# Kernel tuning notes

Measured on AMD Instinct MI355X. Metric: run time of the kernel, lower is better.

The kernel has to match this reference:

```python
import jax, jax.numpy as jnp
import numpy as np

NEG_SLOPE = 0.2
LN_EPS = 1e-5


def gat_conv(x, edge_index, W, att_src, att_dst, bias, heads, out_ch, concat):
    """PyG-style GATConv with add_self_loops=True, eval mode (no dropout)."""
    N = x.shape[0]
    loop = jnp.arange(N, dtype=edge_index.dtype)
    src = jnp.concatenate([edge_index[0], loop])
    dst = jnp.concatenate([edge_index[1], loop])
    h = (x @ W).reshape(N, heads, out_ch)                      # [N,H,C]
    a_src = jnp.sum(h * att_src, axis=-1)                      # [N,H]
    a_dst = jnp.sum(h * att_dst, axis=-1)                      # [N,H]
    e = jax.nn.leaky_relu(a_src[src] + a_dst[dst], NEG_SLOPE)  # [E,H]
    emax = jax.ops.segment_max(e, dst, num_segments=N)         # [N,H]
    ex = jnp.exp(e - emax[dst])
    denom = jax.ops.segment_sum(ex, dst, num_segments=N)       # [N,H]
    alpha = ex / denom[dst]                                    # [E,H]
    msg = h[src] * alpha[..., None]                            # [E,H,C]
    out = jax.ops.segment_sum(msg, dst, num_segments=N)        # [N,H,C]
    out = out.reshape(N, heads * out_ch) if concat else out.mean(axis=1)
    return out + bias


def layer_norm(x, w, b):
    mu = x.mean(-1, keepdims=True)
    var = jnp.mean((x - mu) ** 2, -1, keepdims=True)
    return (x - mu) * jax.lax.rsqrt(var + LN_EPS) * w + b


def setup_inputs() -> dict:
    key = jax.random.key(0)
    ks = jax.random.split(key, 16)
    N, E, R = 50000, 800000, 16
    node_dim, res_dim, hidden, heads = 128, 64, 64, 2
    s = lambda fan: 1.0 / np.sqrt(fan)
    return {
        "x": jax.random.normal(ks[0], (N, node_dim), jnp.float32),
        "edge_index": jax.random.randint(ks[1], (2, E), 0, N, jnp.int64),
        "resource_features": jax.random.normal(ks[2], (N, R, res_dim), jnp.float32),
        "W1": jax.random.normal(ks[3], (node_dim, heads * hidden), jnp.float32) * s(node_dim),
        "att_src1": jax.random.normal(ks[4], (heads, hidden), jnp.float32) * s(hidden),
        "att_dst1": jax.random.normal(ks[5], (heads, hidden), jnp.float32) * s(hidden),
        "b1": jnp.zeros((heads * hidden,), jnp.float32),
        "W2": jax.random.normal(ks[6], (heads * hidden, hidden), jnp.float32) * s(heads * hidden),
        "att_src2": jax.random.normal(ks[7], (1, hidden), jnp.float32) * s(hidden),
        "att_dst2": jax.random.normal(ks[8], (1, hidden), jnp.float32) * s(hidden),
        "b2": jnp.zeros((hidden,), jnp.float32),
        "ln_w": jnp.ones((hidden,), jnp.float32),
        "ln_b": jnp.zeros((hidden,), jnp.float32),
        "res_W": jax.random.normal(ks[9], (res_dim, hidden), jnp.float32) * s(res_dim),
        "res_b": jnp.zeros((hidden,), jnp.float32),
    }


def reference(x, edge_index, resource_features, W1, att_src1, att_dst1, b1,
              W2, att_src2, att_dst2, b2, ln_w, ln_b, res_W, res_b):
    hidden = W2.shape[1]
    heads = att_src1.shape[0]
    h = jax.nn.elu(gat_conv(x, edge_index, W1, att_src1, att_dst1, b1,
                            heads, hidden, concat=True))
    h = gat_conv(h, edge_index, W2, att_src2, att_dst2, b2,
                 1, hidden, concat=False)
    h = layer_norm(h, ln_w, ln_b)                              # [N, hidden]
    R = resource_features.shape[1]
    x_expanded = jnp.broadcast_to(h[:, None, :], (h.shape[0], R, hidden))
    res_emb = jax.nn.elu(resource_features @ res_W + res_b)    # [N,R,hidden]
    return jnp.concatenate([x_expanded, res_emb], axis=-1)     # [N,R,2*hidden]
```

## Files before the change

### kernel.cpp

```cpp
#include <hip/hip_runtime.h>
#include <hip/hip_bf16.h>
#include <math.h>

#define LEAKY_SLOPE 0.2f
#define LN_EPS 1e-5f

typedef __attribute__((ext_vector_type(4))) float f32x4;
typedef __attribute__((ext_vector_type(8))) short short8;

__device__ __forceinline__ float leaky_relu(float x) { return x >= 0.f ? x : LEAKY_SLOPE * x; }
__device__ __forceinline__ float elu1(float x) { return x > 0.f ? x : expm1f(x); }
__device__ __forceinline__ short f2bf(float f) {
    union { __hip_bfloat16 b; short s; } u;
    u.b = __float2bfloat16(f);
    return u.s;
}
__device__ __forceinline__ float bflo(unsigned u) { union { unsigned i; float f; } x; x.i = u << 16; return x.f; }
__device__ __forceinline__ float bfhi(unsigned u) { union { unsigned i; float f; } x; x.i = u & 0xffff0000u; return x.f; }
__device__ __forceinline__ float sbf(short s) { union { unsigned i; float f; } x; x.i = ((unsigned)(unsigned short)s) << 16; return x.f; }
__device__ __forceinline__ unsigned fkey(float f) {
    unsigned b = __float_as_uint(f);
    return b ^ (unsigned)(((int)b >> 31) | 0x80000000);
}
__device__ __forceinline__ float funkey(unsigned k) {
    unsigned b = (k & 0x80000000u) ? (k ^ 0x80000000u) : ~k;
    return __uint_as_float(b);
}

#define DETECT_IS64(ei, E)                                              \
    __shared__ int s_is64;                                              \
    {                                                                   \
        if (threadIdx.x < 64) {                                         \
            int v = (threadIdx.x < (E)) ? ((const int*)(ei))[2 * threadIdx.x + 1] : 0; \
            unsigned long long b = __ballot(v != 0);                    \
            if (threadIdx.x == 0) s_is64 = (b == 0ULL);                 \
        }                                                               \
        __syncthreads();                                                \
    }

#define SUBW1 130
#define DEGB 512
__global__ __launch_bounds__(256) void k_fat1(
    const float* __restrict__ x, const float* __restrict__ W1,
    const float* __restrict__ att_s, const float* __restrict__ att_d,
    short* __restrict__ h1, float* __restrict__ a_src, float* __restrict__ a_dst,
    unsigned* __restrict__ amax, int N,
    const void* __restrict__ ei, int E, int* __restrict__ deg,
    const float* __restrict__ resW, short* __restrict__ rwb, int nbG)
{
    if ((int)blockIdx.x >= nbG) {
        const int b0 = (int)blockIdx.x - nbG;
        if (b0 == 0) {
            for (int idx = threadIdx.x; idx < 4096; idx += 256) {
                int f = idx >> 9, lane = (idx >> 3) & 63, j = idx & 7;
                int kk = f >> 2, nc = f & 3;
                int k = kk * 32 + (lane >> 4) * 8 + j;
                int col = nc * 16 + (lane & 15);
                rwb[idx] = f2bf(resW[k * 64 + col]);
            }
        }
        DETECT_IS64(ei, E)
        const int is64 = s_is64;
        for (int e = b0 * 256 + threadIdx.x; e < E; e += DEGB * 256) {
            int d = is64 ? (int)((const long long*)ei)[(size_t)E + e] : ((const int*)ei)[(size_t)E + e];
            atomicAdd(&deg[d], 1);
        }
        return;
    }
    __shared__ short WT[16 * SUBW1 * 8];
    __shared__ float sb[64 * 4];
    __shared__ float wm[8];
    const int t = threadIdx.x;
    const int w = t >> 6, l = t & 63, lr = l & 15, lk = l >> 4;
    const int n0 = blockIdx.x * 64;
    for (int idx = t; idx < 16384; idx += 256) {
        int k = idx >> 7, col = idx & 127;
        WT[((k >> 3) * SUBW1 + col) * 8 + (k & 7)] = f2bf(W1[idx]);
    }
    sb[t] = 0.f;
    __syncthreads();

    f32x4 acc[4][2];
    #pragma unroll
    for (int mt = 0; mt < 4; ++mt)
        #pragma unroll
        for (int nt = 0; nt < 2; ++nt) acc[mt][nt] = (f32x4){0.f, 0.f, 0.f, 0.f};

    #pragma unroll
    for (int ks = 0; ks < 4; ++ks) {
        short8 bfr[2];
        #pragma unroll
        for (int nt = 0; nt < 2; ++nt) {
            int col = w * 32 + nt * 16 + lr;
            int kk = ks * 4 + lk;
            bfr[nt] = *(const short8*)&WT[(kk * SUBW1 + col) * 8];
        }
        #pragma unroll
        for (int mt = 0; mt < 4; ++mt) {
            int row = n0 + mt * 16 + lr; if (row >= N) row = N - 1;
            const float* ap = x + (size_t)row * 128 + ks * 32 + lk * 8;
            float4 u0 = *(const float4*)ap;
            float4 u1 = *(const float4*)(ap + 4);
            short8 af;
            af[0] = f2bf(u0.x); af[1] = f2bf(u0.y); af[2] = f2bf(u0.z); af[3] = f2bf(u0.w);
            af[4] = f2bf(u1.x); af[5] = f2bf(u1.y); af[6] = f2bf(u1.z); af[7] = f2bf(u1.w);
            acc[mt][0] = __builtin_amdgcn_mfma_f32_16x16x32_bf16(af, bfr[0], acc[mt][0], 0, 0, 0);
            acc[mt][1] = __builtin_amdgcn_mfma_f32_16x16x32_bf16(af, bfr[1], acc[mt][1], 0, 0, 0);
        }
    }

    const int head = w >> 1;
    float asv[2], adv[2];
    #pragma unroll
    for (int nt = 0; nt < 2; ++nt) {
        int ci = (w & 1) * 32 + nt * 16 + lr;
        asv[nt] = att_s[head * 64 + ci];
        adv[nt] = att_d[head * 64 + ci];
    }
    #pragma unroll
    for (int mt = 0; mt < 4; ++mt) {
        #pragma unroll
        for (int i = 0; i < 4; ++i) {
            float ps = acc[mt][0][i] * asv[0] + acc[mt][1][i] * asv[1];
            float pd = acc[mt][0][i] * adv[0] + acc[mt][1][i] * adv[1];
            #pragma unroll
            for (int o = 1; o < 16; o <<= 1) { ps += __shfl_xor(ps, o); pd += __shfl_xor(pd, o); }
            int rl = mt * 16 + lk * 4 + i;
            if (lr == 0) {
                atomicAdd(&sb[rl * 4 + head], ps);
                atomicAdd(&sb[rl * 4 + 2 + head], pd);
            }
            int row = n0 + rl;
            if (row < N) {
                h1[(size_t)row * 128 + w * 32 + lr]      = f2bf(acc[mt][0][i]);
                h1[(size_t)row * 128 + w * 32 + 16 + lr] = f2bf(acc[mt][1][i]);
            }
        }
    }
    __syncthreads();
    int nl = t >> 2, q = t & 3, n = n0 + nl;
    float v = sb[t];
    bool ok = (n < N);
    if (ok) {
        if (q == 0) a_src[n * 2 + 0] = v;
        else if (q == 1) a_src[n * 2 + 1] = v;
        else if (q == 2) a_dst[n * 2 + 0] = v;
        else a_dst[n * 2 + 1] = v;
    }
    float m0 = (ok && q == 0) ? v : -1e30f;
    float m1 = (ok && q == 1) ? v : -1e30f;
    #pragma unroll
    for (int o = 32; o; o >>= 1) { m0 = fmaxf(m0, __shfl_xor(m0, o)); m1 = fmaxf(m1, __shfl_xor(m1, o)); }
    if (l == 0) { wm[w] = m0; wm[4 + w] = m1; }
    __syncthreads();
    if (t == 0) {
        float M0 = fmaxf(fmaxf(wm[0], wm[1]), fmaxf(wm[2], wm[3]));
        float M1 = fmaxf(fmaxf(wm[4], wm[5]), fmaxf(wm[6], wm[7]));
        atomicMax(&amax[0], fkey(M0));
        atomicMax(&amax[1], fkey(M1));
    }
}

__global__ __launch_bounds__(256) void k_bsum(const int* __restrict__ deg, int* __restrict__ bsum, int n)
{
    __shared__ int ws[4];
    const int base = blockIdx.x * 1024;
    int s = 0;
    for (int j = threadIdx.x; j < 1024; j += 256) {
        int i = base + j;
        s += (i < n) ? deg[i] : 0;
    }
    #pragma unroll
    for (int o = 32; o; o >>= 1) s += __shfl_down(s, o);
    if ((threadIdx.x & 63) == 0) ws[threadIdx.x >> 6] = s;
    __syncthreads();
    if (threadIdx.x == 0) bsum[blockIdx.x] = ws[0] + ws[1] + ws[2] + ws[3];
}

__global__ void k_scanb(const int* __restrict__ bsum, int* __restrict__ bbase, int nb)
{
    const int l = threadIdx.x;
    int carry = 0;
    for (int b = 0; b < nb; b += 64) {
        int v = (b + l < nb) ? bsum[b + l] : 0;
        int x = v;
        #pragma unroll
        for (int o = 1; o < 64; o <<= 1) { int y = __shfl_up(x, o); if (l >= o) x += y; }
        if (b + l < nb) bbase[b + l] = carry + x - v;
        carry += __shfl(x, 63);
    }
}

__global__ __launch_bounds__(1024) void k_scan3(const int* __restrict__ deg, const int* __restrict__ bbase,
                                                int* __restrict__ offs, int* __restrict__ cursor, int n)
{
    __shared__ int ws[16];
    const int i = blockIdx.x * 1024 + threadIdx.x;
    const int l = threadIdx.x & 63, w = threadIdx.x >> 6;
    int v = (i < n) ? deg[i] : 0;
    int x = v;
    #pragma unroll
    for (int o = 1; o < 64; o <<= 1) { int y = __shfl_up(x, o); if (l >= o) x += y; }
    if (l == 63) ws[w] = x;
    __syncthreads();
    if (threadIdx.x < 16) {
        int s = ws[threadIdx.x];
        #pragma unroll
        for (int o = 1; o < 16; o <<= 1) { int y = __shfl_up(s, o); if (threadIdx.x >= o) s += y; }
        ws[threadIdx.x] = s;
    }
    __syncthreads();
    int add = (w ? ws[w - 1] : 0) + bbase[blockIdx.x];
    if (i < n) {
        offs[i + 1] = x + add;
        cursor[i] = x + add - v;
    }
    if (blockIdx.x == 0 && threadIdx.x == 0) offs[0] = 0;
}

__global__ __launch_bounds__(256) void k_scatter(const void* __restrict__ ei, int E,
                                                 int* __restrict__ cursor, int* __restrict__ csr_src)
{
    DETECT_IS64(ei, E)
    const int is64 = s_is64;
    for (int e = blockIdx.x * blockDim.x + threadIdx.x; e < E; e += gridDim.x * blockDim.x) {
        int s, d;
        if (is64) {
            const long long* p = (const long long*)ei;
            s = (int)p[e]; d = (int)p[(size_t)E + e];
        } else {
            const int* p = (const int*)ei;
            s = p[e]; d = p[(size_t)E + e];
        }
        int pos = atomicAdd(&cursor[d], 1);
        csr_src[pos] = s;
    }
}

__global__ __launch_bounds__(256) void k_layer1(
    const short* __restrict__ h1, const float* __restrict__ a_s, const float* __restrict__ a_d,
    const int* __restrict__ offs, const int* __restrict__ csr,
    const float* __restrict__ b1, const unsigned* __restrict__ amax,
    short* __restrict__ h1a, int N,
    const float* __restrict__ res, const short* __restrict__ rwb,
    const float* __restrict__ resb, float* __restrict__ out)
{
    const int w = threadIdx.x >> 6, l = threadIdx.x & 63;
    const int n = blockIdx.x * 4 + w;
    if (n >= N) return;
    const float2 adp = *(const float2*)&a_d[2 * n];
    const float2 asp = *(const float2*)&a_s[2 * n];
    const float C0 = leaky_relu(funkey(amax[0]) + adp.x);
    const float C1 = leaky_relu(funkey(amax[1]) + adp.y);
    const float es0 = leaky_relu(asp.x + adp.x) - C0;
    const float es1 = leaky_relu(asp.y + adp.y) - C1;
    const int hsel = l >> 5;
    const int o0 = offs[n], o1 = offs[n + 1];

    float den0 = 0.f, den1 = 0.f;
    float cl0 = 0.f, ch0 = 0.f, cl1 = 0.f, ch1 = 0.f;
    float cl2 = 0.f, ch2 = 0.f, cl3 = 0.f, ch3 = 0.f;
    for (int base = o0; base < o1; base += 64) {
        const int cnt = min(64, o1 - base);
        int sidx = 0; float p0 = 0.f, p1 = 0.f;
        if (l < cnt) {
            sidx = csr[base + l];
            float2 av = *(const float2*)&a_s[2 * sidx];
            p0 = __expf(leaky_relu(av.x + adp.x) - C0);
            p1 = __expf(leaky_relu(av.y + adp.y) - C1);
        }
        den0 += p0; den1 += p1;
        int j = 0;
        for (; j + 4 <= cnt; j += 4) {
            int s0 = __shfl(sidx, j),     s1 = __shfl(sidx, j + 1);
            int s2 = __shfl(sidx, j + 2), s3 = __shfl(sidx, j + 3);
            float q00 = __shfl(p0, j),     q10 = __shfl(p1, j);
            float q01 = __shfl(p0, j + 1), q11 = __shfl(p1, j + 1);
            float q02 = __shfl(p0, j + 2), q12 = __shfl(p1, j + 2);
            float q03 = __shfl(p0, j + 3), q13 = __shfl(p1, j + 3);
            unsigned u0 = *(const unsigned*)(h1 + (size_t)s0 * 128 + 2 * l);
            unsigned u1 = *(const unsigned*)(h1 + (size_t)s1 * 128 + 2 * l);
            unsigned u2 = *(const unsigned*)(h1 + (size_t)s2 * 128 + 2 * l);
            unsigned u3 = *(const unsigned*)(h1 + (size_t)s3 * 128 + 2 * l);
            float w0 = hsel ? q10 : q00, w1 = hsel ? q11 : q01;
            float w2 = hsel ? q12 : q02, w3 = hsel ? q13 : q03;
            cl0 += w0 * bflo(u0); ch0 += w0 * bfhi(u0);
            cl1 += w1 * bflo(u1); ch1 += w1 * bfhi(u1);
            cl2 += w2 * bflo(u2); ch2 += w2 * bfhi(u2);
            cl3 += w3 * bflo(u3); ch3 += w3 * bfhi(u3);
        }
        for (; j < cnt; ++j) {
            int sa = __shfl(sidx, j);
            float qa0 = __shfl(p0, j), qa1 = __shfl(p1, j);
            unsigned ua = *(const unsigned*)(h1 + (size_t)sa * 128 + 2 * l);
            float wa = hsel ? qa1 : qa0;
            cl0 += wa * bflo(ua); ch0 += wa * bfhi(ua);
        }
    }
    #pragma unroll
    for (int o = 32; o; o >>= 1) { den0 += __shfl_xor(den0, o); den1 += __shfl_xor(den1, o); }
    const float psf0 = __expf(es0), psf1 = __expf(es1);
    const float inv0 = 1.f / (den0 + psf0), inv1 = 1.f / (den1 + psf1);

    unsigned us = *(const unsigned*)(h1 + (size_t)n * 128 + 2 * l);
    const float psf = hsel ? psf1 : psf0;
    float acc0 = cl0 + cl1 + cl2 + cl3 + psf * bflo(us);
    float acc1 = ch0 + ch1 + ch2 + ch3 + psf * bfhi(us);
    const float invh = hsel ? inv1 : inv0;
    float2 bv = *(const float2*)&b1[2 * l];
    float v0 = elu1(acc0 * invh + bv.x);
    float v1 = elu1(acc1 * invh + bv.y);
    unsigned up = ((unsigned)(unsigned short)f2bf(v0)) | (((unsigned)(unsigned short)f2bf(v1)) << 16);
    *(unsigned*)(h1a + (size_t)n * 128 + 2 * l) = up;

    __builtin_amdgcn_sched_barrier(0);
    {
        const int lr = l & 15, lk = l >> 4;
        const float* rp = res + (size_t)n * 1024 + lr * 64 + lk * 8;
        const f32x4 f0 = __builtin_nontemporal_load((const f32x4*)(rp));
        const f32x4 f1 = __builtin_nontemporal_load((const f32x4*)(rp + 4));
        const f32x4 f2 = __builtin_nontemporal_load((const f32x4*)(rp + 32));
        const f32x4 f3 = __builtin_nontemporal_load((const f32x4*)(rp + 36));
        short8 fa0, fa1;
        fa0[0] = f2bf(f0[0]); fa0[1] = f2bf(f0[1]); fa0[2] = f2bf(f0[2]); fa0[3] = f2bf(f0[3]);
        fa0[4] = f2bf(f1[0]); fa0[5] = f2bf(f1[1]); fa0[6] = f2bf(f1[2]); fa0[7] = f2bf(f1[3]);
        fa1[0] = f2bf(f2[0]); fa1[1] = f2bf(f2[1]); fa1[2] = f2bf(f2[2]); fa1[3] = f2bf(f2[3]);
        fa1[4] = f2bf(f3[0]); fa1[5] = f2bf(f3[1]); fa1[6] = f2bf(f3[2]); fa1[7] = f2bf(f3[3]);
        const short8* rw8 = (const short8*)rwb;
        float* ob = out + (size_t)n * 2048;
        #pragma unroll
        for (int nc = 0; nc < 4; ++nc) {
            f32x4 a = (f32x4){0.f, 0.f, 0.f, 0.f};
            a = __builtin_amdgcn_mfma_f32_16x16x32_bf16(fa0, rw8[nc * 64 + l], a, 0, 0, 0);
            a = __builtin_amdgcn_mfma_f32_16x16x32_bf16(fa1, rw8[(4 + nc) * 64 + l], a, 0, 0, 0);
            const float rb = resb[nc * 16 + lr];
            #pragma unroll
            for (int ii = 0; ii < 4; ++ii)
                __builtin_nontemporal_store(elu1(a[ii] + rb), ob + (lk * 4 + ii) * 128 + 64 + nc * 16 + lr);
        }
    }
}

#define SUBW2 66
__global__ __launch_bounds__(256) void k_gemm2m(
    const short* __restrict__ h1a, const float* __restrict__ W2,
    const float* __restrict__ att_s, const float* __restrict__ att_d,
    short* __restrict__ h2, float* __restrict__ a_src, float* __restrict__ a_dst,
    unsigned* __restrict__ amax, int N)
{
    __shared__ short WT[16 * SUBW2 * 8];
    __shared__ float sb[64 * 2];
    __shared__ float wm[4];
    const int t = threadIdx.x;
    const int w = t >> 6, l = t & 63, lr = l & 15, lk = l >> 4;
    const int n0 = blockIdx.x * 64;
    for (int idx = t; idx < 8192; idx += 256) {
        int k = idx >> 6, col = idx & 63;
        WT[((k >> 3) * SUBW2 + col) * 8 + (k & 7)] = f2bf(W2[idx]);
    }
    if (t < 128) sb[t] = 0.f;
    __syncthreads();

    f32x4 acc[4];
    #pragma unroll
    for (int mt = 0; mt < 4; ++mt) acc[mt] = (f32x4){0.f, 0.f, 0.f, 0.f};

    #pragma unroll
    for (int ks = 0; ks < 4; ++ks) {
        short8 bfr = *(const short8*)&WT[((ks * 4 + lk) * SUBW2 + w * 16 + lr) * 8];
        #pragma unroll
        for (int mt = 0; mt < 4; ++mt) {
            int row = n0 + mt * 16 + lr; if (row >= N) row = N - 1;
            short8 af = *(const short8*)(h1a + (size_t)row * 128 + ks * 32 + lk * 8);
            acc[mt] = __builtin_amdgcn_mfma_f32_16x16x32_bf16(af, bfr, acc[mt], 0, 0, 0);
        }
    }

    const float asv = att_s[w * 16 + lr], adv = att_d[w * 16 + lr];
    #pragma unroll
    for (int mt = 0; mt < 4; ++mt) {
        #pragma unroll
        for (int i = 0; i < 4; ++i) {
            float ps = acc[mt][i] * asv;
            float pd = acc[mt][i] * adv;
            #pragma unroll
            for (int o = 1; o < 16; o <<= 1) { ps += __shfl_xor(ps, o); pd += __shfl_xor(pd, o); }
            int rl = mt * 16 + lk * 4 + i;
            if (lr == 0) {
                atomicAdd(&sb[rl * 2 + 0], ps);
                atomicAdd(&sb[rl * 2 + 1], pd);
            }
            int row = n0 + rl;
            if (row < N) h2[(size_t)row * 64 + w * 16 + lr] = f2bf(acc[mt][i]);
        }
    }
    __syncthreads();
    float v = (t < 128) ? sb[t] : -1e30f;
    int n = n0 + (t >> 1);
    bool ok = (t < 128) && (n < N);
    if (ok) {
        if (t & 1) a_dst[n] = v;
        else       a_src[n] = v;
    }
    float m0 = (ok && !(t & 1)) ? v : -1e30f;
    #pragma unroll
    for (int o = 32; o; o >>= 1) m0 = fmaxf(m0, __shfl_xor(m0, o));
    if (l == 0) wm[w] = m0;
    __syncthreads();
    if (t == 0) {
        float M0 = fmaxf(fmaxf(wm[0], wm[1]), fmaxf(wm[2], wm[3]));
        atomicMax(&amax[0], fkey(M0));
    }
}

#define NPT 2
__global__ __launch_bounds__(256) void k_tail(
    const short* __restrict__ h2, const float* __restrict__ a_s, const float* __restrict__ a_d,
    const int* __restrict__ offs, const int* __restrict__ csr,
    const float* __restrict__ b2, const float* __restrict__ lnw, const float* __restrict__ lnb,
    const unsigned* __restrict__ amax, float* __restrict__ out, int N)
{
    const int w = threadIdx.x >> 6, l = threadIdx.x & 63;
    const int lr = l & 15, lk = l >> 4;
    const int nbase = (blockIdx.x * 4 + w) * NPT;
    if (nbase >= N) return;
    const float b2l = b2[l], lnwl = lnw[l], lnbl = lnb[l];
    const float Am = funkey(amax[0]);

    for (int i = 0; i < NPT; ++i) {
        const int n = nbase + i;
        if (n >= N) break;
        const float adv = a_d[n];
        const float C = leaky_relu(Am + adv);
        const float es = leaky_relu(a_s[n] + adv) - C;
        const int o0 = offs[n], o1 = offs[n + 1];
        float den = 0.f, a0 = 0.f, a1 = 0.f, a2 = 0.f, a3 = 0.f;
        for (int base = o0; base < o1; base += 64) {
            const int cnt = min(64, o1 - base);
            int sidx = 0; float pv = 0.f;
            if (l < cnt) {
                sidx = csr[base + l];
                pv = __expf(leaky_relu(a_s[sidx] + adv) - C);
            }
            den += pv;
            int j = 0;
            for (; j + 4 <= cnt; j += 4) {
                int s0 = __shfl(sidx, j),     s1 = __shfl(sidx, j + 1);
                int s2 = __shfl(sidx, j + 2), s3 = __shfl(sidx, j + 3);
                float q0 = __shfl(pv, j),     q1 = __shfl(pv, j + 1);
                float q2 = __shfl(pv, j + 2), q3 = __shfl(pv, j + 3);
                a0 += q0 * sbf(h2[(size_t)s0 * 64 + l]);
                a1 += q1 * sbf(h2[(size_t)s1 * 64 + l]);
                a2 += q2 * sbf(h2[(size_t)s2 * 64 + l]);
                a3 += q3 * sbf(h2[(size_t)s3 * 64 + l]);
            }
            for (; j < cnt; ++j) {
                int sa = __shfl(sidx, j);
                float qa = __shfl(pv, j);
                a0 += qa * sbf(h2[(size_t)sa * 64 + l]);
            }
        }
        #pragma unroll
        for (int o = 32; o; o >>= 1) den += __shfl_xor(den, o);
        const float psf = __expf(es);
        const float inv = 1.f / (den + psf);
        float o = (a0 + a1 + a2 + a3 + psf * sbf(h2[(size_t)n * 64 + l])) * inv + b2l;
        float mu = o;
        #pragma unroll
        for (int off = 32; off; off >>= 1) mu += __shfl_xor(mu, off);
        mu *= (1.f / 64.f);
        float d = o - mu;
        float vv = d * d;
        #pragma unroll
        for (int off = 32; off; off >>= 1) vv += __shfl_xor(vv, off);
        vv *= (1.f / 64.f);
        const float hl = d * rsqrtf(vv + LN_EPS) * lnwl + lnbl;
        f32x4 hv;
        #pragma unroll
        for (int j = 0; j < 4; ++j) hv[j] = __shfl(hl, lr * 4 + j);
        float* ob = out + (size_t)n * 2048;
        #pragma unroll
        for (int ii = 0; ii < 4; ++ii)
            __builtin_nontemporal_store(hv, (f32x4*)(ob + (lk + 4 * ii) * 128 + lr * 4));
    }
}

extern "C" void kernel_launch(void* const* d_in, const int* in_sizes, int n_in,
                              void* d_out, int out_size, void* d_ws, size_t ws_size,
                              hipStream_t stream)
{
    const float* x   = (const float*)d_in[0];
    const void*  ei  = d_in[1];
    const float* res = (const float*)d_in[2];
    const float* W1  = (const float*)d_in[3];
    const float* as1 = (const float*)d_in[4];
    const float* ad1 = (const float*)d_in[5];
    const float* b1  = (const float*)d_in[6];
    const float* W2  = (const float*)d_in[7];
    const float* as2 = (const float*)d_in[8];
    const float* ad2 = (const float*)d_in[9];
    const float* b2  = (const float*)d_in[10];
    const float* lnw = (const float*)d_in[11];
    const float* lnb = (const float*)d_in[12];
    const float* rW  = (const float*)d_in[13];
    const float* rb  = (const float*)d_in[14];
    float* out = (float*)d_out;

    const int N = in_sizes[0] / 128;
    const int E = in_sizes[1] / 2;
    const int nb = (N + 1023) / 1024;
    const int nbG = (N + 63) / 64;

    char* base = (char*)d_ws;
    size_t off = 0;
    auto alloc = [&](size_t bytes) -> void* {
        void* p = base + off;
        off = (off + bytes + 255) & ~(size_t)255;
        return p;
    };
    short* h1    = (short*)alloc((size_t)N * 128 * 2);
    short* h1a   = (short*)alloc((size_t)N * 128 * 2);
    short* h2    = (short*)alloc((size_t)N * 64 * 2);
    float* a_s1  = (float*)alloc((size_t)N * 2 * 4);
    float* a_d1  = (float*)alloc((size_t)N * 2 * 4);
    float* a_s2  = (float*)alloc((size_t)N * 4);
    float* a_d2  = (float*)alloc((size_t)N * 4);
    int* deg     = (int*)alloc((size_t)(N + 8) * 4);
    int* offs    = (int*)alloc((size_t)(N + 1) * 4);
    int* cursor  = (int*)alloc((size_t)N * 4);
    int* csr_src = (int*)alloc((size_t)E * 4);
    int* bsum    = (int*)alloc((size_t)nb * 4);
    int* bbase   = (int*)alloc((size_t)nb * 4);
    short* rwb   = (short*)alloc(4096 * 2);
    unsigned* amax1 = (unsigned*)(deg + N);
    unsigned* amax2 = (unsigned*)(deg + N + 2);

    (void)hipMemsetAsync(deg, 0, (size_t)(N + 8) * 4, stream);
    k_fat1<<<nbG + DEGB, 256, 0, stream>>>(x, W1, as1, ad1, h1, a_s1, a_d1, amax1, N, ei, E, deg, rW, rwb, nbG);
    k_bsum<<<nb, 256, 0, stream>>>(deg, bsum, N);
    k_scanb<<<1, 64, 0, stream>>>(bsum, bbase, nb);
    k_scan3<<<nb, 1024, 0, stream>>>(deg, bbase, offs, cursor, N);
    k_scatter<<<512, 256, 0, stream>>>(ei, E, cursor, csr_src);
    k_layer1<<<(N + 3) / 4, 256, 0, stream>>>(h1, a_s1, a_d1, offs, csr_src, b1, amax1, h1a, N,
                                              res, rwb, rb, out);
    k_gemm2m<<<(N + 63) / 64, 256, 0, stream>>>(h1a, W2, as2, ad2, h2, a_s2, a_d2, amax2, N);
    k_tail<<<(N + NPT * 4 - 1) / (NPT * 4), 256, 0, stream>>>(h2, a_s2, a_d2, offs, csr_src, b2, lnw, lnb,
                                                              amax2, out, N);
}
```

Measured before the change: 344.7 us.

## Fuse layer-2 GEMM into layer-1 aggregation and fold block-scan into scan3

Removes the separate k_gemm2m kernel and the h1a intermediate buffer. Each wave in k_layer1 now computes its node's 64-wide h2 row through shuffles against a bf16 transposed W2 that k_fat1 prepares. The same wave also computes a_s2/a_d2 and does a per-node atomicMax. The k_scanb launch is removed because each k_scan3 block now sums its preceding block totals itself. k_tail drops from two nodes per wave to one. These changes save launches and an N×128 bf16 round trip. In exchange they add per-wave scalar FMA work in place of MFMA, more shuffles, and many more atomics on amax2.

```diff
diff --git a/kernel.cpp b/kernel.cpp
--- a/kernel.cpp
+++ b/kernel.cpp
@@ -46,7 +46,8 @@
     short* __restrict__ h1, float* __restrict__ a_src, float* __restrict__ a_dst,
     unsigned* __restrict__ amax, int N,
     const void* __restrict__ ei, int E, int* __restrict__ deg,
-    const float* __restrict__ resW, short* __restrict__ rwb, int nbG)
+    const float* __restrict__ resW, short* __restrict__ rwb,
+    const float* __restrict__ W2, short* __restrict__ w2t, int nbG)
 {
     if ((int)blockIdx.x >= nbG) {
         const int b0 = (int)blockIdx.x - nbG;
@@ -57,6 +58,10 @@
                 int k = kk * 32 + (lane >> 4) * 8 + j;
                 int col = nc * 16 + (lane & 15);
                 rwb[idx] = f2bf(resW[k * 64 + col]);
+            }
+            for (int idx = threadIdx.x; idx < 8192; idx += 256) {
+                int l = idx >> 7, k = idx & 127;
+                w2t[idx] = f2bf(W2[k * 64 + l]);
             }
         }
         DETECT_IS64(ei, E)
@@ -177,26 +182,21 @@
     if (threadIdx.x == 0) bsum[blockIdx.x] = ws[0] + ws[1] + ws[2] + ws[3];
 }
 
-__global__ void k_scanb(const int* __restrict__ bsum, int* __restrict__ bbase, int nb)
-{
-    const int l = threadIdx.x;
-    int carry = 0;
-    for (int b = 0; b < nb; b += 64) {
-        int v = (b + l < nb) ? bsum[b + l] : 0;
-        int x = v;
-        #pragma unroll
-        for (int o = 1; o < 64; o <<= 1) { int y = __shfl_up(x, o); if (l >= o) x += y; }
-        if (b + l < nb) bbase[b + l] = carry + x - v;
-        carry += __shfl(x, 63);
-    }
-}
-
-__global__ __launch_bounds__(1024) void k_scan3(const int* __restrict__ deg, const int* __restrict__ bbase,
-                                                int* __restrict__ offs, int* __restrict__ cursor, int n)
+__global__ __launch_bounds__(1024) void k_scan3(const int* __restrict__ deg, const int* __restrict__ bsum,
+                                                int* __restrict__ offs, int* __restrict__ cursor,
+                                                int n, int nb)
 {
     __shared__ int ws[16];
+    __shared__ int bb;
     const int i = blockIdx.x * 1024 + threadIdx.x;
     const int l = threadIdx.x & 63, w = threadIdx.x >> 6;
+    if (threadIdx.x < 64) {
+        int v = 0;
+        for (int b = l; b < (int)blockIdx.x; b += 64) v += (b < nb) ? bsum[b] : 0;
+        #pragma unroll
+        for (int o = 32; o; o >>= 1) v += __shfl_xor(v, o);
+        if (l == 0) bb = v;
+    }
     int v = (i < n) ? deg[i] : 0;
     int x = v;
     #pragma unroll
@@ -210,7 +210,7 @@
         ws[threadIdx.x] = s;
     }
     __syncthreads();
-    int add = (w ? ws[w - 1] : 0) + bbase[blockIdx.x];
+    int add = (w ? ws[w - 1] : 0) + bb;
     if (i < n) {
         offs[i + 1] = x + add;
         cursor[i] = x + add - v;
@@ -240,10 +240,12 @@
 __global__ __launch_bounds__(256) void k_layer1(
     const short* __restrict__ h1, const float* __restrict__ a_s, const float* __restrict__ a_d,
     const int* __restrict__ offs, const int* __restrict__ csr,
-    const float* __restrict__ b1, const unsigned* __restrict__ amax,
-    short* __restrict__ h1a, int N,
+    const float* __restrict__ b1, const unsigned* __restrict__ amax, int N,
     const float* __restrict__ res, const short* __restrict__ rwb,
-    const float* __restrict__ resb, float* __restrict__ out)
+    const float* __restrict__ resb, float* __restrict__ out,
+    const short* __restrict__ w2t, const float* __restrict__ att_s2, const float* __restrict__ att_d2,
+    short* __restrict__ h2, float* __restrict__ a_s2, float* __restrict__ a_d2,
+    unsigned* __restrict__ amax2)
 {
     const int w = threadIdx.x >> 6, l = threadIdx.x & 63;
     const int n = blockIdx.x * 4 + w;
@@ -308,19 +310,42 @@
     float acc1 = ch0 + ch1 + ch2 + ch3 + psf * bfhi(us);
     const float invh = hsel ? inv1 : inv0;
     float2 bv = *(const float2*)&b1[2 * l];
-    float v0 = elu1(acc0 * invh + bv.x);
-    float v1 = elu1(acc1 * invh + bv.y);
-    unsigned up = ((unsigned)(unsigned short)f2bf(v0)) | (((unsigned)(unsigned short)f2bf(v1)) << 16);
-    *(unsigned*)(h1a + (size_t)n * 128 + 2 * l) = up;
+    const float v0 = elu1(acc0 * invh + bv.x);
+    const float v1 = elu1(acc1 * invh + bv.y);
 
     __builtin_amdgcn_sched_barrier(0);
+    const int lr = l & 15, lk = l >> 4;
+    const float* rp = res + (size_t)n * 1024 + lr * 64 + lk * 8;
+    const f32x4 f0 = __builtin_nontemporal_load((const f32x4*)(rp));
+    const f32x4 f1 = __builtin_nontemporal_load((const f32x4*)(rp + 4));
+    const f32x4 f2 = __builtin_nontemporal_load((const f32x4*)(rp + 32));
+    const f32x4 f3 = __builtin_nontemporal_load((const f32x4*)(rp + 36));
+
     {
-        const int lr = l & 15, lk = l >> 4;
-        const float* rp = res + (size_t)n * 1024 + lr * 64 + lk * 8;
-        const f32x4 f0 = __builtin_nontemporal_load((const f32x4*)(rp));
-        const f32x4 f1 = __builtin_nontemporal_load((const f32x4*)(rp + 4));
-        const f32x4 f2 = __builtin_nontemporal_load((const f32x4*)(rp + 32));
-        const f32x4 f3 = __builtin_nontemporal_load((const f32x4*)(rp + 36));
+        float h2v = 0.f;
+        #pragma unroll
+        for (int j = 0; j < 16; ++j) {
+            short8 w8 = *(const short8*)(w2t + l * 128 + j * 8);
+            #pragma unroll
+            for (int m = 0; m < 4; ++m) {
+                float h0 = __shfl(v0, 4 * j + m);
+                float h1v = __shfl(v1, 4 * j + m);
+                h2v += h0 * sbf(w8[2 * m]) + h1v * sbf(w8[2 * m + 1]);
+            }
+        }
+        h2[(size_t)n * 64 + l] = f2bf(h2v);
+        float ps = h2v * att_s2[l];
+        float pd = h2v * att_d2[l];
+        #pragma unroll
+        for (int o = 32; o; o >>= 1) { ps += __shfl_xor(ps, o); pd += __shfl_xor(pd, o); }
+        if (l == 0) {
+            a_s2[n] = ps;
+            a_d2[n] = pd;
+            atomicMax(&amax2[0], fkey(ps));
+        }
+    }
+
+    {
         short8 fa0, fa1;
         fa0[0] = f2bf(f0[0]); fa0[1] = f2bf(f0[1]); fa0[2] = f2bf(f0[2]); fa0[3] = f2bf(f0[3]);
         fa0[4] = f2bf(f1[0]); fa0[5] = f2bf(f1[1]); fa0[6] = f2bf(f1[2]); fa0[7] = f2bf(f1[3]);
@@ -341,79 +366,6 @@
     }
 }
 
-#define SUBW2 66
-__global__ __launch_bounds__(256) void k_gemm2m(
-    const short* __restrict__ h1a, const float* __restrict__ W2,
-    const float* __restrict__ att_s, const float* __restrict__ att_d,
-    short* __restrict__ h2, float* __restrict__ a_src, float* __restrict__ a_dst,
-    unsigned* __restrict__ amax, int N)
-{
-    __shared__ short WT[16 * SUBW2 * 8];
-    __shared__ float sb[64 * 2];
-    __shared__ float wm[4];
-    const int t = threadIdx.x;
-    const int w = t >> 6, l = t & 63, lr = l & 15, lk = l >> 4;
-    const int n0 = blockIdx.x * 64;
-    for (int idx = t; idx < 8192; idx += 256) {
-        int k = idx >> 6, col = idx & 63;
-        WT[((k >> 3) * SUBW2 + col) * 8 + (k & 7)] = f2bf(W2[idx]);
-    }
-    if (t < 128) sb[t] = 0.f;
-    __syncthreads();
-
-    f32x4 acc[4];
-    #pragma unroll
-    for (int mt = 0; mt < 4; ++mt) acc[mt] = (f32x4){0.f, 0.f, 0.f, 0.f};
-
-    #pragma unroll
-    for (int ks = 0; ks < 4; ++ks) {
-        short8 bfr = *(const short8*)&WT[((ks * 4 + lk) * SUBW2 + w * 16 + lr) * 8];
-        #pragma unroll
-        for (int mt = 0; mt < 4; ++mt) {
-            int row = n0 + mt * 16 + lr; if (row >= N) row = N - 1;
-            short8 af = *(const short8*)(h1a + (size_t)row * 128 + ks * 32 + lk * 8);
-            acc[mt] = __builtin_amdgcn_mfma_f32_16x16x32_bf16(af, bfr, acc[mt], 0, 0, 0);
-        }
-    }
-
-    const float asv = att_s[w * 16 + lr], adv = att_d[w * 16 + lr];
-    #pragma unroll
-    for (int mt = 0; mt < 4; ++mt) {
-        #pragma unroll
-        for (int i = 0; i < 4; ++i) {
-            float ps = acc[mt][i] * asv;
-            float pd = acc[mt][i] * adv;
-            #pragma unroll
-            for (int o = 1; o < 16; o <<= 1) { ps += __shfl_xor(ps, o); pd += __shfl_xor(pd, o); }
-            int rl = mt * 16 + lk * 4 + i;
-            if (lr == 0) {
-                atomicAdd(&sb[rl * 2 + 0], ps);
-                atomicAdd(&sb[rl * 2 + 1], pd);
-            }
-            int row = n0 + rl;
-            if (row < N) h2[(size_t)row * 64 + w * 16 + lr] = f2bf(acc[mt][i]);
-        }
-    }
-    __syncthreads();
-    float v = (t < 128) ? sb[t] : -1e30f;
-    int n = n0 + (t >> 1);
-    bool ok = (t < 128) && (n < N);
-    if (ok) {
-        if (t & 1) a_dst[n] = v;
-        else       a_src[n] = v;
-    }
-    float m0 = (ok && !(t & 1)) ? v : -1e30f;
-    #pragma unroll
-    for (int o = 32; o; o >>= 1) m0 = fmaxf(m0, __shfl_xor(m0, o));
-    if (l == 0) wm[w] = m0;
-    __syncthreads();
-    if (t == 0) {
-        float M0 = fmaxf(fmaxf(wm[0], wm[1]), fmaxf(wm[2], wm[3]));
-        atomicMax(&amax[0], fkey(M0));
-    }
-}
-
-#define NPT 2
 __global__ __launch_bounds__(256) void k_tail(
     const short* __restrict__ h2, const float* __restrict__ a_s, const float* __restrict__ a_d,
     const int* __restrict__ offs, const int* __restrict__ csr,
@@ -422,67 +374,63 @@
 {
     const int w = threadIdx.x >> 6, l = threadIdx.x & 63;
     const int lr = l & 15, lk = l >> 4;
-    const int nbase = (blockIdx.x * 4 + w) * NPT;
-    if (nbase >= N) return;
+    const int n = blockIdx.x * 4 + w;
+    if (n >= N) return;
     const float b2l = b2[l], lnwl = lnw[l], lnbl = lnb[l];
     const float Am = funkey(amax[0]);
 
-    for (int i = 0; i < NPT; ++i) {
-        const int n = nbase + i;
-        if (n >= N) break;
-        const float adv = a_d[n];
-        const float C = leaky_relu(Am + adv);
-        const float es = leaky_relu(a_s[n] + adv) - C;
-        const int o0 = offs[n], o1 = offs[n + 1];
-        float den = 0.f, a0 = 0.f, a1 = 0.f, a2 = 0.f, a3 = 0.f;
-        for (int base = o0; base < o1; base += 64) {
-            const int cnt = min(64, o1 - base);
-            int sidx = 0; float pv = 0.f;
-            if (l < cnt) {
-                sidx = csr[base + l];
-                pv = __expf(leaky_relu(a_s[sidx] + adv) - C);
-            }
-            den += pv;
-            int j = 0;
-            for (; j + 4 <= cnt; j += 4) {
-                int s0 = __shfl(sidx, j),     s1 = __shfl(sidx, j + 1);
-                int s2 = __shfl(sidx, j + 2), s3 = __shfl(sidx, j + 3);
-                float q0 = __shfl(pv, j),     q1 = __shfl(pv, j + 1);
-                float q2 = __shfl(pv, j + 2), q3 = __shfl(pv, j + 3);
-                a0 += q0 * sbf(h2[(size_t)s0 * 64 + l]);
-                a1 += q1 * sbf(h2[(size_t)s1 * 64 + l]);
-                a2 += q2 * sbf(h2[(size_t)s2 * 64 + l]);
-                a3 += q3 * sbf(h2[(size_t)s3 * 64 + l]);
-            }
-            for (; j < cnt; ++j) {
-                int sa = __shfl(sidx, j);
-                float qa = __shfl(pv, j);
-                a0 += qa * sbf(h2[(size_t)sa * 64 + l]);
-            }
-        }
-        #pragma unroll
-        for (int o = 32; o; o >>= 1) den += __shfl_xor(den, o);
-        const float psf = __expf(es);
-        const float inv = 1.f / (den + psf);
-        float o = (a0 + a1 + a2 + a3 + psf * sbf(h2[(size_t)n * 64 + l])) * inv + b2l;
-        float mu = o;
-        #pragma unroll
-        for (int off = 32; off; off >>= 1) mu += __shfl_xor(mu, off);
-        mu *= (1.f / 64.f);
-        float d = o - mu;
-        float vv = d * d;
-        #pragma unroll
-        for (int off = 32; off; off >>= 1) vv += __shfl_xor(vv, off);
-        vv *= (1.f / 64.f);
-        const float hl = d * rsqrtf(vv + LN_EPS) * lnwl + lnbl;
-        f32x4 hv;
-        #pragma unroll
-        for (int j = 0; j < 4; ++j) hv[j] = __shfl(hl, lr * 4 + j);
-        float* ob = out + (size_t)n * 2048;
-        #pragma unroll
-        for (int ii = 0; ii < 4; ++ii)
-            __builtin_nontemporal_store(hv, (f32x4*)(ob + (lk + 4 * ii) * 128 + lr * 4));
-    }
+    const float adv = a_d[n];
+    const float C = leaky_relu(Am + adv);
+    const float es = leaky_relu(a_s[n] + adv) - C;
+    const int o0 = offs[n], o1 = offs[n + 1];
+    float den = 0.f, a0 = 0.f, a1 = 0.f, a2 = 0.f, a3 = 0.f;
+    for (int base = o0; base < o1; base += 64) {
+        const int cnt = min(64, o1 - base);
+        int sidx = 0; float pv = 0.f;
+        if (l < cnt) {
+            sidx = csr[base + l];
+            pv = __expf(leaky_relu(a_s[sidx] + adv) - C);
+        }
+        den += pv;
+        int j = 0;
+        for (; j + 4 <= cnt; j += 4) {
+            int s0 = __shfl(sidx, j),     s1 = __shfl(sidx, j + 1);
+            int s2 = __shfl(sidx, j + 2), s3 = __shfl(sidx, j + 3);
+            float q0 = __shfl(pv, j),     q1 = __shfl(pv, j + 1);
+            float q2 = __shfl(pv, j + 2), q3 = __shfl(pv, j + 3);
+            a0 += q0 * sbf(h2[(size_t)s0 * 64 + l]);
+            a1 += q1 * sbf(h2[(size_t)s1 * 64 + l]);
+            a2 += q2 * sbf(h2[(size_t)s2 * 64 + l]);
+            a3 += q3 * sbf(h2[(size_t)s3 * 64 + l]);
+        }
+        for (; j < cnt; ++j) {
+            int sa = __shfl(sidx, j);
+            float qa = __shfl(pv, j);
+            a0 += qa * sbf(h2[(size_t)sa * 64 + l]);
+        }
+    }
+    #pragma unroll
+    for (int o = 32; o; o >>= 1) den += __shfl_xor(den, o);
+    const float psf = __expf(es);
+    const float inv = 1.f / (den + psf);
+    float o = (a0 + a1 + a2 + a3 + psf * sbf(h2[(size_t)n * 64 + l])) * inv + b2l;
+    float mu = o;
+    #pragma unroll
+    for (int off = 32; off; off >>= 1) mu += __shfl_xor(mu, off);
+    mu *= (1.f / 64.f);
+    float d = o - mu;
+    float vv = d * d;
+    #pragma unroll
+    for (int off = 32; off; off >>= 1) vv += __shfl_xor(vv, off);
+    vv *= (1.f / 64.f);
+    const float hl = d * rsqrtf(vv + LN_EPS) * lnwl + lnbl;
+    f32x4 hv;
+    #pragma unroll
+    for (int j = 0; j < 4; ++j) hv[j] = __shfl(hl, lr * 4 + j);
+    float* ob = out + (size_t)n * 2048;
+    #pragma unroll
+    for (int ii = 0; ii < 4; ++ii)
+        __builtin_nontemporal_store(hv, (f32x4*)(ob + (lk + 4 * ii) * 128 + lr * 4));
 }
 
 extern "C" void kernel_launch(void* const* d_in, const int* in_sizes, int n_in,
@@ -519,7 +467,6 @@
         return p;
     };
     short* h1    = (short*)alloc((size_t)N * 128 * 2);
-    short* h1a   = (short*)alloc((size_t)N * 128 * 2);
     short* h2    = (short*)alloc((size_t)N * 64 * 2);
     float* a_s1  = (float*)alloc((size_t)N * 2 * 4);
     float* a_d1  = (float*)alloc((size_t)N * 2 * 4);
@@ -530,20 +477,19 @@
     int* cursor  = (int*)alloc((size_t)N * 4);
     int* csr_src = (int*)alloc((size_t)E * 4);
     int* bsum    = (int*)alloc((size_t)nb * 4);
-    int* bbase   = (int*)alloc((size_t)nb * 4);
     short* rwb   = (short*)alloc(4096 * 2);
+    short* w2t   = (short*)alloc(8192 * 2);
     unsigned* amax1 = (unsigned*)(deg + N);
     unsigned* amax2 = (unsigned*)(deg + N + 2);
 
     (void)hipMemsetAsync(deg, 0, (size_t)(N + 8) * 4, stream);
-    k_fat1<<<nbG + DEGB, 256, 0, stream>>>(x, W1, as1, ad1, h1, a_s1, a_d1, amax1, N, ei, E, deg, rW, rwb, nbG);
+    k_fat1<<<nbG + DEGB, 256, 0, stream>>>(x, W1, as1, ad1, h1, a_s1, a_d1, amax1, N,
+                                           ei, E, deg, rW, rwb, W2, w2t, nbG);
     k_bsum<<<nb, 256, 0, stream>>>(deg, bsum, N);
-    k_scanb<<<1, 64, 0, stream>>>(bsum, bbase, nb);
-    k_scan3<<<nb, 1024, 0, stream>>>(deg, bbase, offs, cursor, N);
+    k_scan3<<<nb, 1024, 0, stream>>>(deg, bsum, offs, cursor, N, nb);
     k_scatter<<<512, 256, 0, stream>>>(ei, E, cursor, csr_src);
-    k_layer1<<<(N + 3) / 4, 256, 0, stream>>>(h1, a_s1, a_d1, offs, csr_src, b1, amax1, h1a, N,
-                                              res, rwb, rb, out);
-    k_gemm2m<<<(N + 63) / 64, 256, 0, stream>>>(h1a, W2, as2, ad2, h2, a_s2, a_d2, amax2, N);
-    k_tail<<<(N + NPT * 4 - 1) / (NPT * 4), 256, 0, stream>>>(h2, a_s2, a_d2, offs, csr_src, b2, lnw, lnb,
-                                                              amax2, out, N);
-}
+    k_layer1<<<(N + 3) / 4, 256, 0, stream>>>(h1, a_s1, a_d1, offs, csr_src, b1, amax1, N,
+                                              res, rwb, rb, out, w2t, as2, ad2, h2, a_s2, a_d2, amax2);
+    k_tail<<<(N + 3) / 4, 256, 0, stream>>>(h2, a_s2, a_d2, offs, csr_src, b2, lnw, lnb,
+                                            amax2, out, N);
+}
```

After: 770.4 us. +123.5%, slower.
